# Kernel tuning notes

Measured on AMD Instinct MI355X. Metric: run time of the kernel, lower is better.

The kernel has to match this reference:

```python
import jax, jax.numpy as jnp
import numpy as np

D_MODEL = 1024
N_EXPERTS = 8
TOP_K = 2


def setup_inputs() -> dict:
    key = jax.random.key(0)
    ks = jax.random.split(key, 8)
    B, S, D, E, H = 4, 2048, D_MODEL, N_EXPERTS, 4 * D_MODEL
    s1 = 1.0 / np.sqrt(D)
    s2 = 1.0 / np.sqrt(H)
    return {
        "x": jax.random.normal(ks[0], (B, S, D), dtype=jnp.float32),
        "Wg": jax.random.uniform(ks[1], (D, E), jnp.float32, -s1, s1),
        "bg": jax.random.uniform(ks[2], (E,), jnp.float32, -s1, s1),
        "W1": jax.random.uniform(ks[3], (E, D, H), jnp.float32, -s1, s1),
        "b1": jax.random.uniform(ks[4], (E, H), jnp.float32, -s1, s1),
        "W2": jax.random.uniform(ks[5], (E, H, D), jnp.float32, -s2, s2),
        "b2": jax.random.uniform(ks[6], (E, D), jnp.float32, -s2, s2),
    }


def reference(x, Wg, bg, W1, b1, W2, b2):
    B, S, D = x.shape
    E = Wg.shape[1]
    x_flat = x.reshape(-1, D)                      # [T, D]
    logits = x_flat @ Wg + bg                      # [T, E]
    weights = jax.nn.softmax(logits, axis=-1)
    topk_w, topk_idx = jax.lax.top_k(weights, TOP_K)  # [T, K]
    # Per-token combine weight for each expert (sum over k where routed).
    onehot = jax.nn.one_hot(topk_idx, E, dtype=x.dtype)      # [T, K, E]
    combine = jnp.einsum("tk,tke->te", topk_w, onehot)       # [T, E]
    out = jnp.zeros_like(x_flat)
    for e in range(E):  # small fixed loop over experts
        h = jax.nn.gelu(x_flat @ W1[e] + b1[e], approximate=False)
        out = out + combine[:, e:e + 1] * (h @ W2[e] + b2[e])
    return out.reshape(B, S, D)
```

## Files before the change

kernel.cpp:

```cpp
#include <hip/hip_runtime.h>
#include <hip/hip_bf16.h>
#include <math.h>

#define T_TOK 8192
#define DM    1024
#define NE    8
#define HD    4096

typedef __bf16 bf16;
typedef __attribute__((ext_vector_type(8))) __bf16 bf16x8;
typedef __attribute__((ext_vector_type(4))) float  f32x4;

__device__ __forceinline__ void gl_lds16(const void* g, void* l) {
  __builtin_amdgcn_global_load_lds((const __attribute__((address_space(1))) void*)g,
                                   (__attribute__((address_space(3))) void*)l, 16, 0, 0);
}

#define RAW_BARRIER() asm volatile("s_barrier" ::: "memory")
#define WAIT_VM8()    asm volatile("s_waitcnt vmcnt(8)" ::: "memory")

__device__ __forceinline__ int imin(int a, int b) { return a < b ? a : b; }

__global__ void zero_kernel(float* __restrict__ out, int* __restrict__ counts) {
  size_t stride = (size_t)gridDim.x * blockDim.x;
  size_t n4 = (size_t)T_TOK * DM / 4;
  for (size_t i = (size_t)blockIdx.x * blockDim.x + threadIdx.x; i < n4; i += stride) {
    float4 z = {0.f, 0.f, 0.f, 0.f};
    ((float4*)out)[i] = z;
  }
  if (blockIdx.x == 0 && threadIdx.x < NE) counts[threadIdx.x] = 0;
}

__global__ void transpose_cvt_kernel(const float* __restrict__ in, bf16* __restrict__ out,
                                     int R, int C) {
  __shared__ float tile[64][65];
  int e = blockIdx.z;
  int c0 = blockIdx.x * 64, r0 = blockIdx.y * 64;
  int tid = threadIdx.x;
  int lr = tid >> 2, lc = (tid & 3) * 16;
  const float* src = in + ((size_t)e * R + r0 + lr) * C + c0 + lc;
#pragma unroll
  for (int q = 0; q < 4; ++q) {
    float4 v = *(const float4*)(src + q * 4);
    tile[lr][lc + q * 4 + 0] = v.x;
    tile[lr][lc + q * 4 + 1] = v.y;
    tile[lr][lc + q * 4 + 2] = v.z;
    tile[lr][lc + q * 4 + 3] = v.w;
  }
  __syncthreads();
  int oc = tid >> 3;
  int rchunk = tid & 7;
#pragma unroll
  for (int q = 0; q < 2; ++q) {
    int ocq = oc + q * 32;
    bf16x8 o;
#pragma unroll
    for (int k = 0; k < 8; ++k) o[k] = (bf16)tile[rchunk * 8 + k][ocq];
    *(bf16x8*)(out + ((size_t)e * C + c0 + ocq) * R + r0 + rchunk * 8) = o;
  }
}

__global__ void gating_kernel(const float* __restrict__ x, const float* __restrict__ Wg,
                              const float* __restrict__ bg, int* __restrict__ counts,
                              int* __restrict__ tokl, float* __restrict__ wgt,
                              bf16* __restrict__ xb) {
  int t = blockIdx.x * 4 + (threadIdx.x >> 6);
  int lane = threadIdx.x & 63;
  if (t >= T_TOK) return;
  double acc[NE];
#pragma unroll
  for (int e = 0; e < NE; ++e) acc[e] = 0.0;
  const float* xr = x + (size_t)t * DM;
  bf16* xbr = xb + (size_t)t * DM;
  for (int d = lane; d < DM; d += 64) {
    float xv = xr[d];
    xbr[d] = (bf16)xv;
#pragma unroll
    for (int e = 0; e < NE; ++e) acc[e] += (double)xv * (double)Wg[d * NE + e];
  }
#pragma unroll
  for (int e = 0; e < NE; ++e)
    for (int o = 32; o > 0; o >>= 1) acc[e] += __shfl_down(acc[e], o, 64);
  if (lane == 0) {
    float l[NE], w[NE];
    float m = -1e30f;
#pragma unroll
    for (int e = 0; e < NE; ++e) { l[e] = (float)acc[e] + bg[e]; m = fmaxf(m, l[e]); }
    float s = 0.f;
#pragma unroll
    for (int e = 0; e < NE; ++e) { w[e] = expf(l[e] - m); s += w[e]; }
    float inv = 1.f / s;
#pragma unroll
    for (int e = 0; e < NE; ++e) w[e] *= inv;
    int e1 = 0; float v1 = w[0];
#pragma unroll
    for (int e = 1; e < NE; ++e) if (w[e] > v1) { v1 = w[e]; e1 = e; }
    int e2 = -1; float v2 = -1.f;
#pragma unroll
    for (int e = 0; e < NE; ++e) if (e != e1 && w[e] > v2) { v2 = w[e]; e2 = e; }
    int s1 = atomicAdd(&counts[e1], 1);
    tokl[e1 * T_TOK + s1] = t; wgt[e1 * T_TOK + s1] = v1;
    int s2 = atomicAdd(&counts[e2], 1);
    tokl[e2 * T_TOK + s2] = t; wgt[e2 * T_TOK + s2] = v2;
  }
}

__global__ void scan_kernel(const int* __restrict__ counts, int* __restrict__ offsets) {
  if (threadIdx.x == 0 && blockIdx.x == 0) {
    int s = 0;
#pragma unroll
    for (int e = 0; e < NE; ++e) { offsets[e] = s; s += counts[e]; }
    offsets[NE] = s;
  }
}


__global__ __launch_bounds__(512, 2) void gemm1_kernel(
    const bf16* __restrict__ xbf, const bf16* __restrict__ w1t,
    const float* __restrict__ b1, const int* __restrict__ counts,
    const int* __restrict__ offsets, const int* __restrict__ tokl,
    bf16* __restrict__ hbuf, int Hc, int cbase) {
  int bid = blockIdx.x;
  int q = gridDim.x >> 3;
  int L = (bid & 7) * q + (bid >> 3);
  int rt = L & 31;
  int g = L >> 5;
  int NT = Hc >> 8;
  int nt = g % NT, e = g / NT;
  int cnt = counts[e];
  if (rt * 256 >= cnt) return;
  __shared__ __align__(16) bf16 sA[2][256 * 64];
  __shared__ __align__(16) bf16 sB[2][256 * 64];
  int tid = threadIdx.x, lane = tid & 63, w = tid >> 6;
  int ra = tid >> 3;
  int ko = (tid & 7) * 16;
  int kox = ko ^ ((ra & 7) << 4);
  int hoff = offsets[e];
  const char* gA[4];
  const char* gB[4];
#pragma unroll
  for (int s = 0; s < 4; ++s) {
    int r = imin(rt * 256 + ra + s * 64, cnt - 1);
    int t = tokl[e * T_TOK + r];
    gA[s] = (const char*)(xbf + (size_t)t * DM) + kox;
    int col = cbase + nt * 256 + ra + s * 64;
    gB[s] = (const char*)(w1t + ((size_t)e * HD + col) * DM) + kox;
  }
  char* la = (char*)sA;
  char* lb = (char*)sB;
  int dst = w * 1024;
  f32x4 acc[8][4];
#pragma unroll
  for (int i = 0; i < 8; ++i)
#pragma unroll
    for (int j = 0; j < 4; ++j) acc[i][j] = {0.f, 0.f, 0.f, 0.f};
  int mw = (w & 1) * 128, nw = (w >> 1) * 64;
  int swzr = (lane & 7) << 4;
  int colx = ((lane >> 4) * 16) ^ swzr;
  const char* pa0 = (const char*)sA + (mw + (lane & 15)) * 128 + colx;
  const char* pb0 = (const char*)sB + (nw + (lane & 15)) * 128 + colx;
  const char* pa1 = (const char*)sA + (mw + (lane & 15)) * 128 + (colx ^ 64);
  const char* pb1 = (const char*)sB + (nw + (lane & 15)) * 128 + (colx ^ 64);
  const int K = DM / 64;
#pragma unroll
  for (int s = 0; s < 4; ++s) gl_lds16(gA[s], la + s * 8192 + dst);
#pragma unroll
  for (int s = 0; s < 4; ++s) gl_lds16(gB[s], lb + s * 8192 + dst);
  for (int k = 0; k < K; ++k) {
    int nb = (k + 1) & 1;
    int kb = (k + 1 < K) ? (k + 1) * 128 : 0;
    char* lan = la + nb * 32768;
    char* lbn = lb + nb * 32768;
#pragma unroll
    for (int s = 0; s < 4; ++s) gl_lds16(gA[s] + kb, lan + s * 8192 + dst);
#pragma unroll
    for (int s = 0; s < 4; ++s) gl_lds16(gB[s] + kb, lbn + s * 8192 + dst);
    WAIT_VM8();
    RAW_BARRIER();
    int cb = (k & 1) * 32768;
    bf16x8 af[8], bfr[4];
#pragma unroll
    for (int i = 0; i < 8; ++i) af[i] = *(const bf16x8*)(pa0 + cb + i * 2048);
#pragma unroll
    for (int j = 0; j < 4; ++j) bfr[j] = *(const bf16x8*)(pb0 + cb + j * 2048);
#pragma unroll
    for (int i = 0; i < 8; ++i)
#pragma unroll
      for (int j = 0; j < 4; ++j)
        acc[i][j] = __builtin_amdgcn_mfma_f32_16x16x32_bf16(af[i], bfr[j], acc[i][j], 0, 0, 0);
#pragma unroll
    for (int i = 0; i < 8; ++i) af[i] = *(const bf16x8*)(pa1 + cb + i * 2048);
#pragma unroll
    for (int j = 0; j < 4; ++j) bfr[j] = *(const bf16x8*)(pb1 + cb + j * 2048);
#pragma unroll
    for (int i = 0; i < 8; ++i)
#pragma unroll
      for (int j = 0; j < 4; ++j)
        acc[i][j] = __builtin_amdgcn_mfma_f32_16x16x32_bf16(af[i], bfr[j], acc[i][j], 0, 0, 0);
    RAW_BARRIER();
  }
  int colq = lane & 15, rowq = (lane >> 4) * 4;
  int hcol = nt * 256 + nw;
  float b1v[4];
#pragma unroll
  for (int j = 0; j < 4; ++j)
    b1v[j] = b1[(size_t)e * HD + cbase + hcol + j * 16 + colq];
#pragma unroll
  for (int i = 0; i < 8; ++i) {
#pragma unroll
    for (int r = 0; r < 4; ++r) {
      int grow = rt * 256 + mw + i * 16 + rowq + r;
      if (grow < cnt) {
        size_t hrow = (size_t)(hoff + grow) * Hc;
#pragma unroll
        for (int j = 0; j < 4; ++j) {
          float v = acc[i][j][r] + b1v[j];
          float gl = 0.5f * v * (1.f + erff(v * 0.70710678118654752f));
          hbuf[hrow + hcol + j * 16 + colq] = (bf16)gl;
        }
      }
    }
  }
}

__global__ __launch_bounds__(512, 2) void gemm2_kernel(
    const bf16* __restrict__ hbuf, const bf16* __restrict__ w2t,
    const float* __restrict__ b2, const int* __restrict__ counts,
    const int* __restrict__ offsets, const int* __restrict__ tokl,
    const float* __restrict__ wgt, float* __restrict__ out,
    int Hc, int cbase, float b2scale) {
  int bid = blockIdx.x;
  int q = gridDim.x >> 3;
  int L = (bid & 7) * q + (bid >> 3);
  int rt = L & 31;
  int g = L >> 5;
  const int NT = DM / 256;
  int nt = g % NT, e = g / NT;
  int cnt = counts[e];
  if (rt * 256 >= cnt) return;
  __shared__ __align__(16) bf16 sA[2][256 * 64];
  __shared__ __align__(16) bf16 sB[2][256 * 64];
  int tid = threadIdx.x, lane = tid & 63, w = tid >> 6;
  int ra = tid >> 3;
  int ko = (tid & 7) * 16;
  int kox = ko ^ ((ra & 7) << 4);
  int hoff = offsets[e];
  const char* gA[4];
  const char* gB[4];
#pragma unroll
  for (int s = 0; s < 4; ++s) {
    int r = imin(rt * 256 + ra + s * 64, cnt - 1);
    gA[s] = (const char*)(hbuf + (size_t)(hoff + r) * Hc) + kox;
    int col = nt * 256 + ra + s * 64;
    gB[s] = (const char*)(w2t + ((size_t)e * DM + col) * HD + cbase) + kox;
  }
  char* la = (char*)sA;
  char* lb = (char*)sB;
  int dst = w * 1024;
  f32x4 acc[8][4];
#pragma unroll
  for (int i = 0; i < 8; ++i)
#pragma unroll
    for (int j = 0; j < 4; ++j) acc[i][j] = {0.f, 0.f, 0.f, 0.f};
  int mw = (w & 1) * 128, nw = (w >> 1) * 64;
  int swzr = (lane & 7) << 4;
  int colx = ((lane >> 4) * 16) ^ swzr;
  const char* pa0 = (const char*)sA + (mw + (lane & 15)) * 128 + colx;
  const char* pb0 = (const char*)sB + (nw + (lane & 15)) * 128 + colx;
  const char* pa1 = (const char*)sA + (mw + (lane & 15)) * 128 + (colx ^ 64);
  const char* pb1 = (const char*)sB + (nw + (lane & 15)) * 128 + (colx ^ 64);
  const int K = Hc / 64;
#pragma unroll
  for (int s = 0; s < 4; ++s) gl_lds16(gA[s], la + s * 8192 + dst);
#pragma unroll
  for (int s = 0; s < 4; ++s) gl_lds16(gB[s], lb + s * 8192 + dst);
  for (int k = 0; k < K; ++k) {
    int nb = (k + 1) & 1;
    int kb = (k + 1 < K) ? (k + 1) * 128 : 0;
    char* lan = la + nb * 32768;
    char* lbn = lb + nb * 32768;
#pragma unroll
    for (int s = 0; s < 4; ++s) gl_lds16(gA[s] + kb, lan + s * 8192 + dst);
#pragma unroll
    for (int s = 0; s < 4; ++s) gl_lds16(gB[s] + kb, lbn + s * 8192 + dst);
    WAIT_VM8();
    RAW_BARRIER();
    int cb = (k & 1) * 32768;
    bf16x8 af[8], bfr[4];
#pragma unroll
    for (int i = 0; i < 8; ++i) af[i] = *(const bf16x8*)(pa0 + cb + i * 2048);
#pragma unroll
    for (int j = 0; j < 4; ++j) bfr[j] = *(const bf16x8*)(pb0 + cb + j * 2048);
#pragma unroll
    for (int i = 0; i < 8; ++i)
#pragma unroll
      for (int j = 0; j < 4; ++j)
        acc[i][j] = __builtin_amdgcn_mfma_f32_16x16x32_bf16(af[i], bfr[j], acc[i][j], 0, 0, 0);
#pragma unroll
    for (int i = 0; i < 8; ++i) af[i] = *(const bf16x8*)(pa1 + cb + i * 2048);
#pragma unroll
    for (int j = 0; j < 4; ++j) bfr[j] = *(const bf16x8*)(pb1 + cb + j * 2048);
#pragma unroll
    for (int i = 0; i < 8; ++i)
#pragma unroll
      for (int j = 0; j < 4; ++j)
        acc[i][j] = __builtin_amdgcn_mfma_f32_16x16x32_bf16(af[i], bfr[j], acc[i][j], 0, 0, 0);
    RAW_BARRIER();
  }
  int colq = lane & 15, rowq = (lane >> 4) * 4;
  float b2v[4];
#pragma unroll
  for (int j = 0; j < 4; ++j)
    b2v[j] = b2[(size_t)e * DM + nt * 256 + nw + j * 16 + colq] * b2scale;
#pragma unroll
  for (int i = 0; i < 8; ++i) {
#pragma unroll
    for (int r = 0; r < 4; ++r) {
      int grow = rt * 256 + mw + i * 16 + rowq + r;
      if (grow < cnt) {
        float wv = wgt[e * T_TOK + grow];
        int tk = tokl[e * T_TOK + grow];
        float* orow = out + (size_t)tk * DM + nt * 256 + nw;
#pragma unroll
        for (int j = 0; j < 4; ++j)
          atomicAdd(orow + j * 16 + colq, wv * (acc[i][j][r] + b2v[j]));
      }
    }
  }
}

extern "C" void kernel_launch(void* const* d_in, const int* in_sizes, int n_in,
                              void* d_out, int out_size, void* d_ws, size_t ws_size,
                              hipStream_t stream) {
  const float* x  = (const float*)d_in[0];
  const float* Wg = (const float*)d_in[1];
  const float* bg = (const float*)d_in[2];
  const float* W1 = (const float*)d_in[3];
  const float* b1 = (const float*)d_in[4];
  const float* W2 = (const float*)d_in[5];
  const float* b2 = (const float*)d_in[6];
  float* out = (float*)d_out;

  char* ws = (char*)d_ws;
  size_t off = 0;
  auto alloc = [&](size_t bytes) -> void* {
    void* p = ws + off;
    off = (off + bytes + 255) & ~(size_t)255;
    return p;
  };
  int*   counts  = (int*)alloc(NE * 4);
  int*   offsets = (int*)alloc((NE + 1) * 4);
  int*   tokl    = (int*)alloc((size_t)NE * T_TOK * 4);
  float* wgt     = (float*)alloc((size_t)NE * T_TOK * 4);
  bf16*  xbf     = (bf16*)alloc((size_t)T_TOK * DM * 2);
  bf16*  w1t     = (bf16*)alloc((size_t)NE * HD * DM * 2);
  bf16*  w2t     = (bf16*)alloc((size_t)NE * DM * HD * 2);
  size_t remain = ws_size > off ? ws_size - off : 0;
  int Hc = HD;
  while (Hc > 256 && (size_t)2 * T_TOK * Hc * 2 > remain) Hc >>= 1;
  bf16* hbuf = (bf16*)alloc((size_t)2 * T_TOK * Hc * 2);

  zero_kernel<<<4096, 256, 0, stream>>>(out, counts);
  transpose_cvt_kernel<<<dim3(HD / 64, DM / 64, NE), 256, 0, stream>>>(W1, w1t, DM, HD);
  transpose_cvt_kernel<<<dim3(DM / 64, HD / 64, NE), 256, 0, stream>>>(W2, w2t, HD, DM);
  gating_kernel<<<T_TOK / 4, 256, 0, stream>>>(x, Wg, bg, counts, tokl, wgt, xbf);
  scan_kernel<<<1, 64, 0, stream>>>(counts, offsets);

  int nchunk = HD / Hc;
  for (int c = 0; c < nchunk; ++c) {
    gemm1_kernel<<<NE * (Hc / 256) * (T_TOK / 256), 512, 0, stream>>>(
        xbf, w1t, b1, counts, offsets, tokl, hbuf, Hc, c * Hc);
    gemm2_kernel<<<NE * (DM / 256) * (T_TOK / 256), 512, 0, stream>>>(
        hbuf, w2t, b2, counts, offsets, tokl, wgt, out, Hc, c * Hc, c == 0 ? 1.f : 0.f);
  }
}
```

Before: 1.155 ms.

## Split GEMM k-tile into four quadrant phases with interleaved LDS prefetch

Restructures both expert GEMM main loops so each k-tile runs in four phases over 2x2 quadrants of the 256x256 output tile. Global-to-LDS loads for the next tile are issued per half-tile and interleaved with the MFMA phases, using finer vmcnt/lgkmcnt waits, s_setprio around MFMA bursts and sched barriers. Each wave now owns a strided 2x2 set of 64x32 subtiles instead of one contiguous 128x64 block. The aim is better overlap of memory, LDS reads and matrix math, at the cost of more barriers per k-step and fragile hand-tuned wait counts.

Result: faster. 1.112 ms (-3.8%).

```diff
diff --git a/kernel.cpp b/kernel.cpp
--- a/kernel.cpp
+++ b/kernel.cpp
@@ -17,7 +17,8 @@
 }
 
 #define RAW_BARRIER() asm volatile("s_barrier" ::: "memory")
-#define WAIT_VM8()    asm volatile("s_waitcnt vmcnt(8)" ::: "memory")
+#define VMCNT4()      asm volatile("s_waitcnt vmcnt(4)" ::: "memory")
+#define LGKM0()       asm volatile("s_waitcnt lgkmcnt(0)" ::: "memory")
 
 __device__ __forceinline__ int imin(int a, int b) { return a < b ? a : b; }
 
@@ -114,6 +115,65 @@
   }
 }
 
+
+#define LDA_F(IH, CB) \
+  _Pragma("unroll") for (int kh = 0; kh < 2; ++kh) \
+  _Pragma("unroll") for (int i = 0; i < 4; ++i) \
+    af[kh*4+i] = *(const bf16x8*)(Ab + (CB) + (128*(IH) + 64*wm + 16*i + lf) * 128 + (colx ^ (kh*64)));
+
+#define LDB_F(JH, CB) \
+  _Pragma("unroll") for (int kh = 0; kh < 2; ++kh) \
+  _Pragma("unroll") for (int j = 0; j < 2; ++j) \
+    bfr[kh*2+j] = *(const bf16x8*)(Bb + (CB) + (128*(JH) + 32*wn + 16*j + lf) * 128 + (colx ^ (kh*64)));
+
+#define MM_F(IH, JH) \
+  _Pragma("unroll") for (int kh = 0; kh < 2; ++kh) \
+  _Pragma("unroll") for (int i = 0; i < 4; ++i) \
+  _Pragma("unroll") for (int j = 0; j < 2; ++j) \
+    acc[IH][JH][i][j] = __builtin_amdgcn_mfma_f32_16x16x32_bf16(af[kh*4+i], bfr[kh*2+j], acc[IH][JH][i][j], 0, 0, 0);
+
+#define ISSUE_A(H, NBO, KB) do { \
+    gl_lds16(gA[2*(H)] + (KB), Al + (NBO) + (H)*16384 + dst); \
+    gl_lds16(gA[2*(H)+1] + (KB), Al + (NBO) + (H)*16384 + 8192 + dst); \
+  } while (0)
+#define ISSUE_B(H, NBO, KB) do { \
+    gl_lds16(gB[2*(H)] + (KB), Bl + (NBO) + (H)*16384 + dst); \
+    gl_lds16(gB[2*(H)+1] + (KB), Bl + (NBO) + (H)*16384 + 8192 + dst); \
+  } while (0)
+
+#define PH_TAIL(IH, JH) \
+    RAW_BARRIER(); \
+    LGKM0(); __builtin_amdgcn_sched_barrier(0); \
+    __builtin_amdgcn_s_setprio(1); \
+    MM_F(IH, JH); \
+    __builtin_amdgcn_s_setprio(0);
+
+#define KTILE_BODY(CB, NBO, KB) \
+     \
+    LDA_F(0, CB); \
+    LDB_F(0, CB); \
+    ISSUE_A(0, NBO, KB); \
+    PH_TAIL(0, 0) \
+    VMCNT4(); \
+    RAW_BARRIER(); \
+     \
+    LDB_F(1, CB); \
+    ISSUE_B(0, NBO, KB); \
+    PH_TAIL(0, 1) \
+    VMCNT4(); \
+    RAW_BARRIER(); \
+     \
+    LDA_F(1, CB); \
+    LDB_F(0, CB); \
+    ISSUE_B(1, NBO, KB); \
+    PH_TAIL(1, 0) \
+    RAW_BARRIER(); \
+     \
+    LDB_F(1, CB); \
+    ISSUE_A(1, NBO, KB); \
+    PH_TAIL(1, 1) \
+    VMCNT4(); \
+    RAW_BARRIER();
 
 __global__ __launch_bounds__(512, 2) void gemm1_kernel(
     const bf16* __restrict__ xbf, const bf16* __restrict__ w1t,
@@ -132,9 +192,13 @@
   __shared__ __align__(16) bf16 sA[2][256 * 64];
   __shared__ __align__(16) bf16 sB[2][256 * 64];
   int tid = threadIdx.x, lane = tid & 63, w = tid >> 6;
+  int wm = w & 1, wn = w >> 1;
+  int lf = lane & 15;
+  int colx = ((lane >> 4) * 16) ^ ((lane & 7) << 4);
   int ra = tid >> 3;
   int ko = (tid & 7) * 16;
   int kox = ko ^ ((ra & 7) << 4);
+  int dst = w * 1024;
   int hoff = offsets[e];
   const char* gA[4];
   const char* gB[4];
@@ -146,77 +210,56 @@
     int col = cbase + nt * 256 + ra + s * 64;
     gB[s] = (const char*)(w1t + ((size_t)e * HD + col) * DM) + kox;
   }
-  char* la = (char*)sA;
-  char* lb = (char*)sB;
-  int dst = w * 1024;
-  f32x4 acc[8][4];
-#pragma unroll
-  for (int i = 0; i < 8; ++i)
-#pragma unroll
-    for (int j = 0; j < 4; ++j) acc[i][j] = {0.f, 0.f, 0.f, 0.f};
-  int mw = (w & 1) * 128, nw = (w >> 1) * 64;
-  int swzr = (lane & 7) << 4;
-  int colx = ((lane >> 4) * 16) ^ swzr;
-  const char* pa0 = (const char*)sA + (mw + (lane & 15)) * 128 + colx;
-  const char* pb0 = (const char*)sB + (nw + (lane & 15)) * 128 + colx;
-  const char* pa1 = (const char*)sA + (mw + (lane & 15)) * 128 + (colx ^ 64);
-  const char* pb1 = (const char*)sB + (nw + (lane & 15)) * 128 + (colx ^ 64);
+  char* Al = (char*)sA;
+  char* Bl = (char*)sB;
+  const char* Ab = (const char*)sA;
+  const char* Bb = (const char*)sB;
+  f32x4 acc[2][2][4][2];
+#pragma unroll
+  for (int ih = 0; ih < 2; ++ih)
+#pragma unroll
+    for (int jh = 0; jh < 2; ++jh)
+#pragma unroll
+      for (int i = 0; i < 4; ++i)
+#pragma unroll
+        for (int j = 0; j < 2; ++j) acc[ih][jh][i][j] = {0.f, 0.f, 0.f, 0.f};
+  bf16x8 af[8], bfr[4];
   const int K = DM / 64;
-#pragma unroll
-  for (int s = 0; s < 4; ++s) gl_lds16(gA[s], la + s * 8192 + dst);
-#pragma unroll
-  for (int s = 0; s < 4; ++s) gl_lds16(gB[s], lb + s * 8192 + dst);
+  ISSUE_A(0, 0, 0); ISSUE_B(0, 0, 0); ISSUE_B(1, 0, 0); ISSUE_A(1, 0, 0);
+  VMCNT4();
+  RAW_BARRIER();
   for (int k = 0; k < K; ++k) {
-    int nb = (k + 1) & 1;
+    int cb = (k & 1) * 32768;
+    int nbo = ((k + 1) & 1) * 32768;
     int kb = (k + 1 < K) ? (k + 1) * 128 : 0;
-    char* lan = la + nb * 32768;
-    char* lbn = lb + nb * 32768;
-#pragma unroll
-    for (int s = 0; s < 4; ++s) gl_lds16(gA[s] + kb, lan + s * 8192 + dst);
-#pragma unroll
-    for (int s = 0; s < 4; ++s) gl_lds16(gB[s] + kb, lbn + s * 8192 + dst);
-    WAIT_VM8();
-    RAW_BARRIER();
-    int cb = (k & 1) * 32768;
-    bf16x8 af[8], bfr[4];
-#pragma unroll
-    for (int i = 0; i < 8; ++i) af[i] = *(const bf16x8*)(pa0 + cb + i * 2048);
-#pragma unroll
-    for (int j = 0; j < 4; ++j) bfr[j] = *(const bf16x8*)(pb0 + cb + j * 2048);
-#pragma unroll
-    for (int i = 0; i < 8; ++i)
-#pragma unroll
-      for (int j = 0; j < 4; ++j)
-        acc[i][j] = __builtin_amdgcn_mfma_f32_16x16x32_bf16(af[i], bfr[j], acc[i][j], 0, 0, 0);
-#pragma unroll
-    for (int i = 0; i < 8; ++i) af[i] = *(const bf16x8*)(pa1 + cb + i * 2048);
-#pragma unroll
-    for (int j = 0; j < 4; ++j) bfr[j] = *(const bf16x8*)(pb1 + cb + j * 2048);
-#pragma unroll
-    for (int i = 0; i < 8; ++i)
-#pragma unroll
-      for (int j = 0; j < 4; ++j)
-        acc[i][j] = __builtin_amdgcn_mfma_f32_16x16x32_bf16(af[i], bfr[j], acc[i][j], 0, 0, 0);
-    RAW_BARRIER();
+    KTILE_BODY(cb, nbo, kb)
   }
   int colq = lane & 15, rowq = (lane >> 4) * 4;
-  int hcol = nt * 256 + nw;
-  float b1v[4];
-#pragma unroll
-  for (int j = 0; j < 4; ++j)
-    b1v[j] = b1[(size_t)e * HD + cbase + hcol + j * 16 + colq];
-#pragma unroll
-  for (int i = 0; i < 8; ++i) {
-#pragma unroll
-    for (int r = 0; r < 4; ++r) {
-      int grow = rt * 256 + mw + i * 16 + rowq + r;
-      if (grow < cnt) {
-        size_t hrow = (size_t)(hoff + grow) * Hc;
-#pragma unroll
-        for (int j = 0; j < 4; ++j) {
-          float v = acc[i][j][r] + b1v[j];
-          float gl = 0.5f * v * (1.f + erff(v * 0.70710678118654752f));
-          hbuf[hrow + hcol + j * 16 + colq] = (bf16)gl;
+  size_t ebase = (size_t)e * HD + cbase + nt * 256;
+  float b1v[2][2];
+#pragma unroll
+  for (int jh = 0; jh < 2; ++jh)
+#pragma unroll
+    for (int j = 0; j < 2; ++j)
+      b1v[jh][j] = b1[ebase + 128 * jh + 32 * wn + 16 * j + colq];
+#pragma unroll
+  for (int ih = 0; ih < 2; ++ih) {
+#pragma unroll
+    for (int i = 0; i < 4; ++i) {
+#pragma unroll
+      for (int r = 0; r < 4; ++r) {
+        int grow = rt * 256 + 128 * ih + 64 * wm + 16 * i + rowq + r;
+        if (grow < cnt) {
+          size_t hrow = (size_t)(hoff + grow) * Hc + nt * 256;
+#pragma unroll
+          for (int jh = 0; jh < 2; ++jh) {
+#pragma unroll
+            for (int j = 0; j < 2; ++j) {
+              float v = acc[ih][jh][i][j][r] + b1v[jh][j];
+              float gl = 0.5f * v * (1.f + erff(v * 0.70710678118654752f));
+              hbuf[hrow + 128 * jh + 32 * wn + 16 * j + colq] = (bf16)gl;
+            }
+          }
         }
       }
     }
@@ -241,9 +284,13 @@
   __shared__ __align__(16) bf16 sA[2][256 * 64];
   __shared__ __align__(16) bf16 sB[2][256 * 64];
   int tid = threadIdx.x, lane = tid & 63, w = tid >> 6;
+  int wm = w & 1, wn = w >> 1;
+  int lf = lane & 15;
+  int colx = ((lane >> 4) * 16) ^ ((lane & 7) << 4);
   int ra = tid >> 3;
   int ko = (tid & 7) * 16;
   int kox = ko ^ ((ra & 7) << 4);
+  int dst = w * 1024;
   int hoff = offsets[e];
   const char* gA[4];
   const char* gB[4];
@@ -254,76 +301,56 @@
     int col = nt * 256 + ra + s * 64;
     gB[s] = (const char*)(w2t + ((size_t)e * DM + col) * HD + cbase) + kox;
   }
-  char* la = (char*)sA;
-  char* lb = (char*)sB;
-  int dst = w * 1024;
-  f32x4 acc[8][4];
-#pragma unroll
-  for (int i = 0; i < 8; ++i)
-#pragma unroll
-    for (int j = 0; j < 4; ++j) acc[i][j] = {0.f, 0.f, 0.f, 0.f};
-  int mw = (w & 1) * 128, nw = (w >> 1) * 64;
-  int swzr = (lane & 7) << 4;
-  int colx = ((lane >> 4) * 16) ^ swzr;
-  const char* pa0 = (const char*)sA + (mw + (lane & 15)) * 128 + colx;
-  const char* pb0 = (const char*)sB + (nw + (lane & 15)) * 128 + colx;
-  const char* pa1 = (const char*)sA + (mw + (lane & 15)) * 128 + (colx ^ 64);
-  const char* pb1 = (const char*)sB + (nw + (lane & 15)) * 128 + (colx ^ 64);
+  char* Al = (char*)sA;
+  char* Bl = (char*)sB;
+  const char* Ab = (const char*)sA;
+  const char* Bb = (const char*)sB;
+  f32x4 acc[2][2][4][2];
+#pragma unroll
+  for (int ih = 0; ih < 2; ++ih)
+#pragma unroll
+    for (int jh = 0; jh < 2; ++jh)
+#pragma unroll
+      for (int i = 0; i < 4; ++i)
+#pragma unroll
+        for (int j = 0; j < 2; ++j) acc[ih][jh][i][j] = {0.f, 0.f, 0.f, 0.f};
+  bf16x8 af[8], bfr[4];
   const int K = Hc / 64;
-#pragma unroll
-  for (int s = 0; s < 4; ++s) gl_lds16(gA[s], la + s * 8192 + dst);
-#pragma unroll
-  for (int s = 0; s < 4; ++s) gl_lds16(gB[s], lb + s * 8192 + dst);
+  ISSUE_A(0, 0, 0); ISSUE_B(0, 0, 0); ISSUE_B(1, 0, 0); ISSUE_A(1, 0, 0);
+  VMCNT4();
+  RAW_BARRIER();
   for (int k = 0; k < K; ++k) {
-    int nb = (k + 1) & 1;
+    int cb = (k & 1) * 32768;
+    int nbo = ((k + 1) & 1) * 32768;
     int kb = (k + 1 < K) ? (k + 1) * 128 : 0;
-    char* lan = la + nb * 32768;
-    char* lbn = lb + nb * 32768;
-#pragma unroll
-    for (int s = 0; s < 4; ++s) gl_lds16(gA[s] + kb, lan + s * 8192 + dst);
-#pragma unroll
-    for (int s = 0; s < 4; ++s) gl_lds16(gB[s] + kb, lbn + s * 8192 + dst);
-    WAIT_VM8();
-    RAW_BARRIER();
-    int cb = (k & 1) * 32768;
-    bf16x8 af[8], bfr[4];
-#pragma unroll
-    for (int i = 0; i < 8; ++i) af[i] = *(const bf16x8*)(pa0 + cb + i * 2048);
-#pragma unroll
-    for (int j = 0; j < 4; ++j) bfr[j] = *(const bf16x8*)(pb0 + cb + j * 2048);
-#pragma unroll
-    for (int i = 0; i < 8; ++i)
-#pragma unroll
-      for (int j = 0; j < 4; ++j)
-        acc[i][j] = __builtin_amdgcn_mfma_f32_16x16x32_bf16(af[i], bfr[j], acc[i][j], 0, 0, 0);
-#pragma unroll
-    for (int i = 0; i < 8; ++i) af[i] = *(const bf16x8*)(pa1 + cb + i * 2048);
-#pragma unroll
-    for (int j = 0; j < 4; ++j) bfr[j] = *(const bf16x8*)(pb1 + cb + j * 2048);
-#pragma unroll
-    for (int i = 0; i < 8; ++i)
-#pragma unroll
-      for (int j = 0; j < 4; ++j)
-        acc[i][j] = __builtin_amdgcn_mfma_f32_16x16x32_bf16(af[i], bfr[j], acc[i][j], 0, 0, 0);
-    RAW_BARRIER();
+    KTILE_BODY(cb, nbo, kb)
   }
   int colq = lane & 15, rowq = (lane >> 4) * 4;
-  float b2v[4];
-#pragma unroll
-  for (int j = 0; j < 4; ++j)
-    b2v[j] = b2[(size_t)e * DM + nt * 256 + nw + j * 16 + colq] * b2scale;
-#pragma unroll
-  for (int i = 0; i < 8; ++i) {
-#pragma unroll
-    for (int r = 0; r < 4; ++r) {
-      int grow = rt * 256 + mw + i * 16 + rowq + r;
-      if (grow < cnt) {
-        float wv = wgt[e * T_TOK + grow];
-        int tk = tokl[e * T_TOK + grow];
-        float* orow = out + (size_t)tk * DM + nt * 256 + nw;
-#pragma unroll
-        for (int j = 0; j < 4; ++j)
-          atomicAdd(orow + j * 16 + colq, wv * (acc[i][j][r] + b2v[j]));
+  float b2v[2][2];
+#pragma unroll
+  for (int jh = 0; jh < 2; ++jh)
+#pragma unroll
+    for (int j = 0; j < 2; ++j)
+      b2v[jh][j] = b2[(size_t)e * DM + nt * 256 + 128 * jh + 32 * wn + 16 * j + colq] * b2scale;
+#pragma unroll
+  for (int ih = 0; ih < 2; ++ih) {
+#pragma unroll
+    for (int i = 0; i < 4; ++i) {
+#pragma unroll
+      for (int r = 0; r < 4; ++r) {
+        int grow = rt * 256 + 128 * ih + 64 * wm + 16 * i + rowq + r;
+        if (grow < cnt) {
+          float wv = wgt[e * T_TOK + grow];
+          int tk = tokl[e * T_TOK + grow];
+          float* orow = out + (size_t)tk * DM + nt * 256;
+#pragma unroll
+          for (int jh = 0; jh < 2; ++jh) {
+#pragma unroll
+            for (int j = 0; j < 2; ++j)
+              atomicAdd(orow + 128 * jh + 32 * wn + 16 * j + colq,
+                        wv * (acc[ih][jh][i][j][r] + b2v[jh][j]));
+          }
+        }
       }
     }
   }
```
